# Performance work log

Measured on AMD Instinct MI355X. Metric: run time of the kernel, lower is better.

Reference implementation:

```python
import jax, jax.numpy as jnp
import numpy as np

N_NODES = 100000
N_EDGES = 1250000
D_IN, D_HID, D_OUT = 64, 128, 64


def _seg_mean(msg, dst, n):
    # mean aggregation over incoming neighbors (PyG SAGEConv aggr='mean')
    s = jax.ops.segment_sum(msg, dst, num_segments=n)
    cnt = jax.ops.segment_sum(jnp.ones((msg.shape[0], 1), msg.dtype), dst, num_segments=n)
    return s / jnp.maximum(cnt, 1.0)


def setup_inputs() -> dict:
    key = jax.random.key(0)
    ks = jax.random.split(key, 8)
    x = jax.random.normal(ks[0], (N_NODES, D_IN), dtype=jnp.float32)
    edge_index = jax.random.randint(ks[1], (2, N_EDGES), 0, N_NODES, dtype=jnp.int32)
    # SAGEConv params: lin_l (on aggregated neighbors, with bias), lin_r (on root, no bias)
    s1 = 1.0 / np.sqrt(D_IN)
    s2 = 1.0 / np.sqrt(D_HID)
    W1_l = jax.random.normal(ks[2], (D_IN, D_HID), dtype=jnp.float32) * s1
    W1_r = jax.random.normal(ks[3], (D_IN, D_HID), dtype=jnp.float32) * s1
    b1 = jnp.zeros((D_HID,), dtype=jnp.float32)
    W2_l = jax.random.normal(ks[4], (D_HID, D_OUT), dtype=jnp.float32) * s2
    W2_r = jax.random.normal(ks[5], (D_HID, D_OUT), dtype=jnp.float32) * s2
    b2 = jnp.zeros((D_OUT,), dtype=jnp.float32)
    return {"x": x, "edge_index": edge_index, "W1_l": W1_l, "b1": b1, "W1_r": W1_r,
            "W2_l": W2_l, "b2": b2, "W2_r": W2_r}


def reference(x, edge_index, W1_l, b1, W1_r, W2_l, b2, W2_r):
    n = x.shape[0]
    src, dst = edge_index[0], edge_index[1]
    # layer 1: SAGEConv = lin_l(mean_{j in N(i)} x_j) + lin_r(x_i)
    agg1 = _seg_mean(x[src], dst, n)                      # [N, D_IN]
    h = agg1 @ W1_l + b1 + x @ W1_r                       # [N, D_HID]
    h = jax.nn.relu(h)                                    # dropout is identity in eval
    # layer 2
    agg2 = _seg_mean(h[src], dst, n)                      # [N, D_HID]
    out = agg2 @ W2_l + b2 + h @ W2_r                     # [N, D_OUT]
    return out
```

## Files before the change

kernel.cpp:

```cpp
#include <hip/hip_runtime.h>

#define NN 100000
#define NE 1250000

#define NBLK1 320
#define CHUNK 3907
#define NBUK  196
#define CAP   8192

#define SCALE_X 23.0f
#define SCALE_P 24.0f
#define PLANE_B 3200000

typedef __attribute__((ext_vector_type(8))) short short8;
typedef __attribute__((ext_vector_type(4))) float f32x4;

static constexpr size_t I_BH    = 0;
static constexpr size_t I_BT    = 62720;
static constexpr size_t I_BB    = 62976;
static constexpr size_t I_OFFS  = 63232;
static constexpr size_t I_PAIRS = 163236;
static constexpr size_t I_SSRC  = 1413236;
static constexpr size_t B_UBASE = 10652944;
static constexpr size_t B_XB    = 0;
static constexpr size_t B_AGG   = 12800000;
static constexpr size_t B_WF1   = 25600000;
static constexpr size_t B_WF2   = 25632768;
static constexpr size_t B_XQ    = 25665536;
static constexpr size_t B_PQ    = 32065536;

__device__ __forceinline__ float bf2f(unsigned int u16) {
    unsigned int v = u16 << 16;
    return __builtin_bit_cast(float, v);
}
__device__ __forceinline__ unsigned int f2bf(float f) {
    unsigned int u = __builtin_bit_cast(unsigned int, f);
    return (u + 0x7fffu + ((u >> 16) & 1u)) >> 16;
}
__device__ __forceinline__ int f2i8(float f, float scale) {
    float c = fminf(fmaxf(f * scale, -127.f), 127.f);
    return (int)rintf(c);
}

__global__ __launch_bounds__(256) void conv_x(const float* __restrict__ x,
                                              unsigned short* __restrict__ xb,
                                              char* __restrict__ xq)
{
    int t = blockIdx.x * 256 + threadIdx.x;
    int n = t >> 3, c8 = (t & 7) * 8;
    const float* xp = x + (size_t)n * 64 + c8;
    float4 v0 = *(const float4*)(xp);
    float4 v1 = *(const float4*)(xp + 4);
    uint4 o;
    o.x = f2bf(v0.x) | (f2bf(v0.y) << 16);
    o.y = f2bf(v0.z) | (f2bf(v0.w) << 16);
    o.z = f2bf(v1.x) | (f2bf(v1.y) << 16);
    o.w = f2bf(v1.z) | (f2bf(v1.w) << 16);
    *(uint4*)(xb + (size_t)n * 64 + c8) = o;
    uint2 q;
    q.x = (f2i8(v0.x, SCALE_X) & 0xff) | ((f2i8(v0.y, SCALE_X) & 0xff) << 8) |
          ((f2i8(v0.z, SCALE_X) & 0xff) << 16) | ((unsigned)(f2i8(v0.w, SCALE_X) & 0xff) << 24);
    q.y = (f2i8(v1.x, SCALE_X) & 0xff) | ((f2i8(v1.y, SCALE_X) & 0xff) << 8) |
          ((f2i8(v1.z, SCALE_X) & 0xff) << 16) | ((unsigned)(f2i8(v1.w, SCALE_X) & 0xff) << 24);
    *(uint2*)(xq + (size_t)(c8 >> 5) * PLANE_B + (size_t)n * 32 + (c8 & 31)) = q;
}

__global__ __launch_bounds__(256) void prep_w(
    const float* __restrict__ W1l, const float* __restrict__ W1r,
    const float* __restrict__ W2l, const float* __restrict__ W2r,
    unsigned short* __restrict__ Wf1, unsigned short* __restrict__ Wf2)
{
    int i = blockIdx.x * 256 + threadIdx.x;
    if (i >= 16384) return;
    int e    = i & 7;
    int ch   = i >> 3;
    int lrow = ch & 15;
    int lk   = (ch >> 4) & 3;
    int kk   = (ch >> 6) & 3;
    int c    = ch >> 8;
    int j = c * 16 + lrow;
    int k = kk * 32 + lk * 8 + e;
    float w1 = (k < 64) ? W1l[(size_t)k * 128 + j] : W1r[(size_t)(k - 64) * 128 + j];
    Wf1[i] = (unsigned short)f2bf(w1);
    float w2 = (j < 64) ? W2l[(size_t)k * 64 + j] : W2r[(size_t)k * 64 + (j - 64)];
    Wf2[i] = (unsigned short)f2bf(w2);
}

__global__ __launch_bounds__(512) void p0_hist(const int* __restrict__ dstv,
                                               int* __restrict__ blockHist)
{
    __shared__ int hist[NBUK];
    const int t = threadIdx.x, b = blockIdx.x;
    for (int i = t; i < NBUK; i += 512) hist[i] = 0;
    __syncthreads();
    const int start = b * CHUNK;
    const int end   = min(start + CHUNK, NE);
    for (int e = start + t; e < end; e += 512)
        atomicAdd(&hist[dstv[e] >> 9], 1);
    __syncthreads();
    for (int i = t; i < NBUK; i += 512)
        blockHist[(size_t)i * NBLK1 + b] = hist[i];
}

__global__ __launch_bounds__(512) void p_scanA(int* __restrict__ blockHist,
                                               int* __restrict__ bucketTot)
{
    __shared__ int s[512];
    const int b = blockIdx.x, t = threadIdx.x;
    int v = (t < NBLK1) ? blockHist[(size_t)b * NBLK1 + t] : 0;
    s[t] = v;
    __syncthreads();
    for (int d = 1; d < 512; d <<= 1) {
        int x = (t >= d) ? s[t - d] : 0;
        __syncthreads();
        s[t] += x;
        __syncthreads();
    }
    if (t < NBLK1) blockHist[(size_t)b * NBLK1 + t] = s[t] - v;
    if (t == NBLK1 - 1) bucketTot[b] = s[t];
}

__global__ __launch_bounds__(256) void p_scanB(const int* __restrict__ bucketTot,
                                               int* __restrict__ bucketBase,
                                               int* __restrict__ offs)
{
    __shared__ int s[256];
    const int t = threadIdx.x;
    int v = (t < NBUK) ? bucketTot[t] : 0;
    s[t] = v;
    __syncthreads();
    for (int d = 1; d < 256; d <<= 1) {
        int x = (t >= d) ? s[t - d] : 0;
        __syncthreads();
        s[t] += x;
        __syncthreads();
    }
    if (t < NBUK) bucketBase[t] = s[t] - v;
    if (t == 0) { bucketBase[NBUK] = NE; offs[NN] = NE; }
}

__global__ __launch_bounds__(512) void p1_scatter(
    const int* __restrict__ srcv, const int* __restrict__ dstv,
    const int* __restrict__ blockHist, const int* __restrict__ bucketBase,
    int* __restrict__ pairs)
{
    __shared__ int cur[NBUK];
    const int t = threadIdx.x, b = blockIdx.x;
    for (int i = t; i < NBUK; i += 512)
        cur[i] = bucketBase[i] + blockHist[(size_t)i * NBLK1 + b];
    __syncthreads();
    const int start = b * CHUNK;
    const int end   = min(start + CHUNK, NE);
    for (int e = start + t; e < end; e += 512) {
        int d = dstv[e], s = srcv[e];
        int pos = atomicAdd(&cur[d >> 9], 1);
        pairs[pos] = s | ((d & 511) << 17);
    }
}

__global__ __launch_bounds__(1024) void p2_sort(
    const int* __restrict__ pairs, const int* __restrict__ bucketBase,
    int* __restrict__ offs, int* __restrict__ ssrc)
{
    __shared__ int buf[CAP];
    __shared__ int hist[512];
    const int b = blockIdx.x, t = threadIdx.x;
    const int base = bucketBase[b];
    const int m    = bucketBase[b + 1] - base;
    const bool fits = (m <= CAP);

    if (t < 512) hist[t] = 0;
    __syncthreads();
    for (int i = t; i < m; i += 1024) {
        int v = pairs[base + i];
        if (fits) buf[i] = v;
        atomicAdd(&hist[v >> 17], 1);
    }
    __syncthreads();

    int ov = (t < 512) ? hist[t] : 0;
    __syncthreads();
    for (int d = 1; d < 512; d <<= 1) {
        int x = 0;
        if (t < 512 && t >= d) x = hist[t - d];
        __syncthreads();
        if (t < 512) hist[t] += x;
        __syncthreads();
    }
    int excl = 0;
    if (t < 512) excl = hist[t] - ov;
    __syncthreads();
    if (t < 512) {
        hist[t] = excl;
        int n = b * 512 + t;
        if (n < NN) offs[n] = base + excl;
    }
    __syncthreads();
    for (int i = t; i < m; i += 1024) {
        int v = fits ? buf[i] : pairs[base + i];
        int pos = atomicAdd(&hist[v >> 17], 1);
        ssrc[base + pos] = v & 0x1FFFF;
    }
}

template <int FUSE>
__global__ __launch_bounds__(256) void sage_gather(
    const int* __restrict__ offs, const int* __restrict__ ssrc,
    const char* __restrict__ feat,
    const float* __restrict__ b2,
    unsigned short* __restrict__ aggb, float* __restrict__ out)
{
    const int plane = blockIdx.x & 1;
    const int nb    = blockIdx.x >> 1;
    const int tid   = threadIdx.x;
    const int n     = nb * 16 + (tid >> 4);
    const int l     = tid & 15;
    const int par   = l >> 2;
    const int ch    = l & 3;
    const int e0 = offs[n], e1 = offs[n + 1];
    const char* pl = feat + (size_t)plane * PLANE_B;

    int ai[8];
    #pragma unroll
    for (int j = 0; j < 8; ++j) ai[j] = 0;

    int e = e0 + par;
    for (; e + 4 < e1; e += 8) {
        int s0 = ssrc[e], s1 = ssrc[e + 4];
        uint2 u = *(const uint2*)(pl + (size_t)s0 * 32 + ch * 8);
        uint2 v = *(const uint2*)(pl + (size_t)s1 * 32 + ch * 8);
        ai[0] += (int)(signed char)(u.x)       + (int)(signed char)(v.x);
        ai[1] += (int)(signed char)(u.x >> 8)  + (int)(signed char)(v.x >> 8);
        ai[2] += (int)(signed char)(u.x >> 16) + (int)(signed char)(v.x >> 16);
        ai[3] += (int)(signed char)(u.x >> 24) + (int)(signed char)(v.x >> 24);
        ai[4] += (int)(signed char)(u.y)       + (int)(signed char)(v.y);
        ai[5] += (int)(signed char)(u.y >> 8)  + (int)(signed char)(v.y >> 8);
        ai[6] += (int)(signed char)(u.y >> 16) + (int)(signed char)(v.y >> 16);
        ai[7] += (int)(signed char)(u.y >> 24) + (int)(signed char)(v.y >> 24);
    }
    if (e < e1) {
        int s0 = ssrc[e];
        uint2 u = *(const uint2*)(pl + (size_t)s0 * 32 + ch * 8);
        ai[0] += (int)(signed char)(u.x);
        ai[1] += (int)(signed char)(u.x >> 8);
        ai[2] += (int)(signed char)(u.x >> 16);
        ai[3] += (int)(signed char)(u.x >> 24);
        ai[4] += (int)(signed char)(u.y);
        ai[5] += (int)(signed char)(u.y >> 8);
        ai[6] += (int)(signed char)(u.y >> 16);
        ai[7] += (int)(signed char)(u.y >> 24);
    }
    #pragma unroll
    for (int j = 0; j < 8; ++j) ai[j] += __shfl_xor(ai[j], 4);
    #pragma unroll
    for (int j = 0; j < 8; ++j) ai[j] += __shfl_xor(ai[j], 8);
    if (par) return;

    const int dg = e1 - e0;
    const float mul = 1.0f / ((float)(dg > 0 ? dg : 1) *
                              (FUSE == 0 ? SCALE_X : SCALE_P));
    float acc[8];
    #pragma unroll
    for (int j = 0; j < 8; ++j) acc[j] = (float)ai[j] * mul;

    const int cbase = plane * 32 + ch * 8;
    if (FUSE == 0) {
        uint4 o;
        o.x = f2bf(acc[0]) | (f2bf(acc[1]) << 16);
        o.y = f2bf(acc[2]) | (f2bf(acc[3]) << 16);
        o.z = f2bf(acc[4]) | (f2bf(acc[5]) << 16);
        o.w = f2bf(acc[6]) | (f2bf(acc[7]) << 16);
        *(uint4*)(aggb + (size_t)n * 64 + cbase) = o;
    } else {
        float* o = out + (size_t)n * 64 + cbase;
        float4 q0 = *(const float4*)(o);
        float4 q1 = *(const float4*)(o + 4);
        float4 c0 = *(const float4*)(b2 + cbase);
        float4 c1 = *(const float4*)(b2 + cbase + 4);
        *(float4*)(o)     = make_float4(acc[0] + q0.x + c0.x, acc[1] + q0.y + c0.y,
                                        acc[2] + q0.z + c0.z, acc[3] + q0.w + c0.w);
        *(float4*)(o + 4) = make_float4(acc[4] + q1.x + c1.x, acc[5] + q1.y + c1.y,
                                        acc[6] + q1.z + c1.z, acc[7] + q1.w + c1.w);
    }
}

__global__ __launch_bounds__(256) void sage_fused(
    const unsigned short* __restrict__ agg, const unsigned short* __restrict__ xb,
    const unsigned short* __restrict__ Wf1, const unsigned short* __restrict__ Wf2,
    const float* __restrict__ b1,
    char* __restrict__ pq, float* __restrict__ outq)
{
    __shared__ __align__(16) unsigned short sW1[16384];
    __shared__ __align__(16) unsigned short sW2[16384];
    __shared__ __align__(16) unsigned short sh[4][2048];

    const int tid  = threadIdx.x;
    const int lane = tid & 63;
    const int wid  = tid >> 6;
    const int lrow = lane & 15;
    const int lk   = lane >> 4;

    {
        const uint4* g1 = (const uint4*)Wf1;
        const uint4* g2 = (const uint4*)Wf2;
        uint4* s1 = (uint4*)sW1;
        uint4* s2 = (uint4*)sW2;
        #pragma unroll
        for (int i = 0; i < 8; ++i) {
            int idx = tid + i * 256;
            s1[idx] = g1[idx];
            s2[idx] = g2[idx];
        }
    }
    __syncthreads();

    const int rbase = blockIdx.x * 64 + wid * 16;
    int arow = rbase + lrow;
    if (arow >= NN) arow = NN - 1;

    short8 a1[4];
    #pragma unroll
    for (int kk = 0; kk < 4; ++kk) {
        int k0 = kk * 32 + lk * 8;
        const unsigned short* ap = (k0 < 64) ? (agg + (size_t)arow * 64 + k0)
                                             : (xb  + (size_t)arow * 64 + (k0 - 64));
        a1[kk] = *(const short8*)ap;
    }

    const int fragoff = (lk * 16 + lrow) * 8;

    f32x4 acc1[8];
    #pragma unroll
    for (int c = 0; c < 8; ++c) {
        acc1[c] = (f32x4){0.f, 0.f, 0.f, 0.f};
        #pragma unroll
        for (int kk = 0; kk < 4; ++kk) {
            short8 b = *(const short8*)(sW1 + fragoff + c * 2048 + kk * 512);
            acc1[c] = __builtin_amdgcn_mfma_f32_16x16x32_bf16(a1[kk], b, acc1[c], 0, 0, 0);
        }
    }

    unsigned short* myh = &sh[wid][0];
    #pragma unroll
    for (int c = 0; c < 8; ++c) {
        float bv = b1[c * 16 + lrow];
        int chbase = ((2 * c + (lrow >> 3)) * 16 + lk * 4) * 8 + (lrow & 7);
        #pragma unroll
        for (int ri = 0; ri < 4; ++ri) {
            float v = fmaxf(acc1[c][ri] + bv, 0.f);
            myh[chbase + ri * 8] = (unsigned short)f2bf(v);
        }
    }

    short8 a2[4];
    #pragma unroll
    for (int kk = 0; kk < 4; ++kk)
        a2[kk] = *(const short8*)(myh + fragoff + kk * 512);

    f32x4 acc2[8];
    #pragma unroll
    for (int c = 0; c < 8; ++c) {
        acc2[c] = (f32x4){0.f, 0.f, 0.f, 0.f};
        #pragma unroll
        for (int kk = 0; kk < 4; ++kk) {
            short8 b = *(const short8*)(sW2 + fragoff + c * 2048 + kk * 512);
            acc2[c] = __builtin_amdgcn_mfma_f32_16x16x32_bf16(a2[kk], b, acc2[c], 0, 0, 0);
        }
    }

    #pragma unroll
    for (int c = 0; c < 8; ++c) {
        int col = c * 16 + lrow;
        #pragma unroll
        for (int ri = 0; ri < 4; ++ri) {
            int row = rbase + lk * 4 + ri;
            if (row >= NN) continue;
            if (col < 64)
                pq[(size_t)(col >> 5) * PLANE_B + (size_t)row * 32 + (col & 31)] =
                    (char)f2i8(acc2[c][ri], SCALE_P);
            else
                outq[(size_t)row * 64 + (col - 64)] = acc2[c][ri];
        }
    }
}

extern "C" void kernel_launch(void* const* d_in, const int* in_sizes, int n_in,
                              void* d_out, int out_size, void* d_ws, size_t ws_size,
                              hipStream_t stream)
{
    const float* x    = (const float*)d_in[0];
    const int*   ei   = (const int*)d_in[1];
    const float* W1_l = (const float*)d_in[2];
    const float* b1   = (const float*)d_in[3];
    const float* W1_r = (const float*)d_in[4];
    const float* W2_l = (const float*)d_in[5];
    const float* b2   = (const float*)d_in[6];
    const float* W2_r = (const float*)d_in[7];

    float* out = (float*)d_out;
    int*   wi  = (int*)d_ws;
    char*  ub  = (char*)d_ws + B_UBASE;

    const int* srcv = ei;
    const int* dstv = ei + NE;

    int* blockHist  = wi + I_BH;
    int* bucketTot  = wi + I_BT;
    int* bucketBase = wi + I_BB;
    int* offs       = wi + I_OFFS;
    int* pairs      = wi + I_PAIRS;
    int* ssrc       = wi + I_SSRC;
    unsigned short* xb  = (unsigned short*)(ub + B_XB);
    unsigned short* agg = (unsigned short*)(ub + B_AGG);
    unsigned short* Wf1 = (unsigned short*)(ub + B_WF1);
    unsigned short* Wf2 = (unsigned short*)(ub + B_WF2);
    char* xq = ub + B_XQ;
    char* pq = ub + B_PQ;

    conv_x <<<(NN * 8) / 256, 256, 0, stream>>>(x, xb, xq);
    prep_w <<<64, 256, 0, stream>>>(W1_l, W1_r, W2_l, W2_r, Wf1, Wf2);

    p0_hist   <<<NBLK1, 512, 0, stream>>>(dstv, blockHist);
    p_scanA   <<<NBUK, 512, 0, stream>>>(blockHist, bucketTot);
    p_scanB   <<<1, 256, 0, stream>>>(bucketTot, bucketBase, offs);
    p1_scatter<<<NBLK1, 512, 0, stream>>>(srcv, dstv, blockHist, bucketBase, pairs);
    p2_sort   <<<NBUK, 1024, 0, stream>>>(pairs, bucketBase, offs, ssrc);

    sage_gather<0><<<(NN * 32) / 256, 256, 0, stream>>>(offs, ssrc, xq, nullptr, agg, nullptr);

    sage_fused<<<(NN + 63) / 64, 256, 0, stream>>>(agg, xb, Wf1, Wf2, b1, pq, out);

    sage_gather<1><<<(NN * 32) / 256, 256, 0, stream>>>(offs, ssrc, pq, b2, nullptr, out);
}
```

Before: 127.9 us.

## Assign gather feature planes by XCC via atomic tickets and use nontemporal accesses

Each gather block reads its XCC id from a hardware register and claims a node-block index from a per-plane atomic ticket counter, so blocks on even XCCs mostly work on plane 0 and blocks on odd XCCs on plane 1. The goal is to keep each XCC's L2 working set to a single 3.2MB quantized feature plane. Edge-index loads and output stores switch to nontemporal hints so they do not evict the feature data from cache. This adds one global atomic per block, a __syncthreads, and a memset per launch, and it makes block-to-work mapping nondeterministic.

```diff
diff --git a/kernel.cpp b/kernel.cpp
--- a/kernel.cpp
+++ b/kernel.cpp
@@ -11,13 +11,16 @@
 #define SCALE_X 23.0f
 #define SCALE_P 24.0f
 #define PLANE_B 3200000
+#define GNB16   6250
 
 typedef __attribute__((ext_vector_type(8))) short short8;
 typedef __attribute__((ext_vector_type(4))) float f32x4;
+typedef __attribute__((ext_vector_type(4))) unsigned int u32x4;
 
 static constexpr size_t I_BH    = 0;
 static constexpr size_t I_BT    = 62720;
 static constexpr size_t I_BB    = 62976;
+static constexpr size_t I_TKT   = 63224;
 static constexpr size_t I_OFFS  = 63232;
 static constexpr size_t I_PAIRS = 163236;
 static constexpr size_t I_SSRC  = 1413236;
@@ -208,15 +211,29 @@
     const int* __restrict__ offs, const int* __restrict__ ssrc,
     const char* __restrict__ feat,
     const float* __restrict__ b2,
+    int* __restrict__ tkt,
     unsigned short* __restrict__ aggb, float* __restrict__ out)
 {
-    const int plane = blockIdx.x & 1;
-    const int nb    = blockIdx.x >> 1;
-    const int tid   = threadIdx.x;
-    const int n     = nb * 16 + (tid >> 4);
-    const int l     = tid & 15;
-    const int par   = l >> 2;
-    const int ch    = l & 3;
+    __shared__ int s_claim[2];
+    const int tid = threadIdx.x;
+    if (tid == 0) {
+        unsigned int xcc;
+        asm volatile("s_getreg_b32 %0, hwreg(HW_REG_XCC_ID)" : "=s"(xcc));
+        int pl  = (int)(xcc & 1u);
+        int pos = atomicAdd(&tkt[pl], 1);
+        if (pos >= GNB16) { pl ^= 1; pos = atomicAdd(&tkt[pl], 1); }
+        s_claim[0] = pl;
+        s_claim[1] = pos;
+    }
+    __syncthreads();
+    const int plane = s_claim[0];
+    const int nb    = s_claim[1];
+    if (nb >= GNB16) return;
+
+    const int n   = nb * 16 + (tid >> 4);
+    const int l   = tid & 15;
+    const int par = l >> 2;
+    const int ch  = l & 3;
     const int e0 = offs[n], e1 = offs[n + 1];
     const char* pl = feat + (size_t)plane * PLANE_B;
 
@@ -226,7 +243,8 @@
 
     int e = e0 + par;
     for (; e + 4 < e1; e += 8) {
-        int s0 = ssrc[e], s1 = ssrc[e + 4];
+        int s0 = __builtin_nontemporal_load(ssrc + e);
+        int s1 = __builtin_nontemporal_load(ssrc + e + 4);
         uint2 u = *(const uint2*)(pl + (size_t)s0 * 32 + ch * 8);
         uint2 v = *(const uint2*)(pl + (size_t)s1 * 32 + ch * 8);
         ai[0] += (int)(signed char)(u.x)       + (int)(signed char)(v.x);
@@ -239,7 +257,7 @@
         ai[7] += (int)(signed char)(u.y >> 24) + (int)(signed char)(v.y >> 24);
     }
     if (e < e1) {
-        int s0 = ssrc[e];
+        int s0 = __builtin_nontemporal_load(ssrc + e);
         uint2 u = *(const uint2*)(pl + (size_t)s0 * 32 + ch * 8);
         ai[0] += (int)(signed char)(u.x);
         ai[1] += (int)(signed char)(u.x >> 8);
@@ -265,22 +283,24 @@
 
     const int cbase = plane * 32 + ch * 8;
     if (FUSE == 0) {
-        uint4 o;
+        u32x4 o;
         o.x = f2bf(acc[0]) | (f2bf(acc[1]) << 16);
         o.y = f2bf(acc[2]) | (f2bf(acc[3]) << 16);
         o.z = f2bf(acc[4]) | (f2bf(acc[5]) << 16);
         o.w = f2bf(acc[6]) | (f2bf(acc[7]) << 16);
-        *(uint4*)(aggb + (size_t)n * 64 + cbase) = o;
+        __builtin_nontemporal_store(o, (u32x4*)(aggb + (size_t)n * 64 + cbase));
     } else {
         float* o = out + (size_t)n * 64 + cbase;
         float4 q0 = *(const float4*)(o);
         float4 q1 = *(const float4*)(o + 4);
         float4 c0 = *(const float4*)(b2 + cbase);
         float4 c1 = *(const float4*)(b2 + cbase + 4);
-        *(float4*)(o)     = make_float4(acc[0] + q0.x + c0.x, acc[1] + q0.y + c0.y,
-                                        acc[2] + q0.z + c0.z, acc[3] + q0.w + c0.w);
-        *(float4*)(o + 4) = make_float4(acc[4] + q1.x + c1.x, acc[5] + q1.y + c1.y,
-                                        acc[6] + q1.z + c1.z, acc[7] + q1.w + c1.w);
+        f32x4 r0 = {acc[0] + q0.x + c0.x, acc[1] + q0.y + c0.y,
+                    acc[2] + q0.z + c0.z, acc[3] + q0.w + c0.w};
+        f32x4 r1 = {acc[4] + q1.x + c1.x, acc[5] + q1.y + c1.y,
+                    acc[6] + q1.z + c1.z, acc[7] + q1.w + c1.w};
+        __builtin_nontemporal_store(r0, (f32x4*)(o));
+        __builtin_nontemporal_store(r1, (f32x4*)(o + 4));
     }
 }
 
@@ -407,6 +427,7 @@
     int* blockHist  = wi + I_BH;
     int* bucketTot  = wi + I_BT;
     int* bucketBase = wi + I_BB;
+    int* tkt        = wi + I_TKT;
     int* offs       = wi + I_OFFS;
     int* pairs      = wi + I_PAIRS;
     int* ssrc       = wi + I_SSRC;
@@ -417,6 +438,8 @@
     char* xq = ub + B_XQ;
     char* pq = ub + B_PQ;
 
+    (void)hipMemsetAsync(tkt, 0, 16, stream);
+
     conv_x <<<(NN * 8) / 256, 256, 0, stream>>>(x, xb, xq);
     prep_w <<<64, 256, 0, stream>>>(W1_l, W1_r, W2_l, W2_r, Wf1, Wf2);
 
@@ -426,9 +449,9 @@
     p1_scatter<<<NBLK1, 512, 0, stream>>>(srcv, dstv, blockHist, bucketBase, pairs);
     p2_sort   <<<NBUK, 1024, 0, stream>>>(pairs, bucketBase, offs, ssrc);
 
-    sage_gather<0><<<(NN * 32) / 256, 256, 0, stream>>>(offs, ssrc, xq, nullptr, agg, nullptr);
+    sage_gather<0><<<GNB16 * 2, 256, 0, stream>>>(offs, ssrc, xq, nullptr, tkt, agg, nullptr);
 
     sage_fused<<<(NN + 63) / 64, 256, 0, stream>>>(agg, xb, Wf1, Wf2, b1, pq, out);
 
-    sage_gather<1><<<(NN * 32) / 256, 256, 0, stream>>>(offs, ssrc, pq, b2, nullptr, out);
-}
+    sage_gather<1><<<GNB16 * 2, 256, 0, stream>>>(offs, ssrc, pq, b2, tkt + 2, nullptr, out);
+}
```

Measured after the change: 377.6 us, median of 2. 2.95x slower.
